# Kernel tuning notes

Hardware: AMD Instinct MI355X
Metric: run time of the kernel (lower is better)

The kernel has to match this reference:

```python
import jax, jax.numpy as jnp
import numpy as np

BETA = 0.05  # module hardcodes self.beta = 0.05 regardless of init arg
K = 4096
D = 512


def setup_inputs() -> dict:
    key = jax.random.key(0)
    k1, k2 = jax.random.split(key)
    latents = jax.random.normal(k1, (32, 1024, D), dtype=jnp.float32)
    # nn.Embedding weight init: normal_(mean=0.8, std=0.1)
    emb_weight = 0.8 + 0.1 * jax.random.normal(k2, (K, D), dtype=jnp.float32)
    return {"latents": latents, "emb_weight": emb_weight}


def reference(latents, emb_weight):
    B, S, Dm = latents.shape
    flat = latents.reshape(-1, Dm)  # [N, D]
    dist = (jnp.sum(flat * flat, axis=1, keepdims=True)
            + jnp.sum(emb_weight * emb_weight, axis=1)
            - 2.0 * jnp.matmul(flat, emb_weight.T))  # [N, K]
    inds = jnp.argmin(dist, axis=1)  # [N]
    quantized = emb_weight[inds].reshape(B, S, Dm)  # gather instead of one-hot matmul

    commitment_loss = jnp.mean((jax.lax.stop_gradient(quantized) - latents) ** 2)
    embedding_loss = jnp.mean((quantized - jax.lax.stop_gradient(latents)) ** 2)
    vq_loss = commitment_loss * BETA + embedding_loss

    # straight-through estimator
    quantized_st = latents + jax.lax.stop_gradient(quantized - latents)

    N = flat.shape[0]
    avg_probs = jnp.zeros((K,), dtype=latents.dtype).at[inds].add(1.0) / N
    perplexity = jnp.exp(-jnp.sum(avg_probs * jnp.log(avg_probs + 1e-10)))

    output_inds = inds.reshape(B, S)
    return (quantized_st, vq_loss, output_inds, emb_weight, perplexity)
```

## Files before the change

kernel.cpp:

```cpp
#include <hip/hip_runtime.h>
#include <cfloat>
#include <cmath>
#include <climits>
#include <cstdint>

#define N_ROWS   32768
#define D_DIM    512
#define K_CODES  4096

#define EPS_GAP  0.008f
#define CAND_WIN 0.02f
#define FLAG_CAP 12000

typedef short s16x8 __attribute__((ext_vector_type(8)));
typedef float f32x4 __attribute__((ext_vector_type(4)));


__device__ __forceinline__ short f2bf_rne(float x) {
    unsigned u = __float_as_uint(x);
    unsigned r = (u + 0x7fffu + ((u >> 16) & 1u)) >> 16;
    return (short)r;
}
__device__ __forceinline__ float bf2f(short b) {
    return __uint_as_float(((unsigned)(unsigned short)b) << 16);
}

__device__ __forceinline__ void gld16(const short* g, short* l) {
    __builtin_amdgcn_global_load_lds(
        reinterpret_cast<const __attribute__((address_space(1))) unsigned int*>(
            reinterpret_cast<uintptr_t>(g)),
        reinterpret_cast<__attribute__((address_space(3))) unsigned int*>(
            (unsigned int)(reinterpret_cast<uintptr_t>(l))),
        16, 0, 0);
}

__device__ __forceinline__ float np_block128_sq(const float* p) {
    float P[16];
    #pragma unroll
    for (int l = 0; l < 16; ++l) {
        float s0 = __fmul_rn(p[0 * 16 + l], p[0 * 16 + l]);
        float s1 = __fmul_rn(p[1 * 16 + l], p[1 * 16 + l]);
        float s2 = __fmul_rn(p[2 * 16 + l], p[2 * 16 + l]);
        float s3 = __fmul_rn(p[3 * 16 + l], p[3 * 16 + l]);
        float s4 = __fmul_rn(p[4 * 16 + l], p[4 * 16 + l]);
        float s5 = __fmul_rn(p[5 * 16 + l], p[5 * 16 + l]);
        float s6 = __fmul_rn(p[6 * 16 + l], p[6 * 16 + l]);
        float s7 = __fmul_rn(p[7 * 16 + l], p[7 * 16 + l]);
        float a01 = __fadd_rn(s0, s1);
        float a23 = __fadd_rn(s2, s3);
        float a45 = __fadd_rn(s4, s5);
        float a67 = __fadd_rn(s6, s7);
        P[l] = __fadd_rn(__fadd_rn(a01, a23), __fadd_rn(a45, a67));
    }
    float T3[8];
    #pragma unroll
    for (int k = 0; k < 8; ++k) T3[k] = __fadd_rn(P[k], P[k + 8]);
    float T6[4];
    #pragma unroll
    for (int k = 0; k < 4; ++k) T6[k] = __fadd_rn(T3[k], T3[k + 4]);
    return __fadd_rn(__fadd_rn(__fadd_rn(T6[0], T6[1]), T6[2]), T6[3]);
}
__device__ __forceinline__ float np_sum512_sq(const float* p) {
    float B0 = np_block128_sq(p);
    float B1 = np_block128_sq(p + 128);
    float B2 = np_block128_sq(p + 256);
    float B3 = np_block128_sq(p + 384);
    return __fadd_rn(__fadd_rn(B0, B1), __fadd_rn(B2, B3));
}

__global__ void vq_convert(const float* __restrict__ emb,
                           short* __restrict__ emb_hi, short* __restrict__ emb_lo) {
    int i = blockIdx.x * 256 + threadIdx.x;
    size_t base = (size_t)i * 8;
    float4 a = *(const float4*)(emb + base);
    float4 b = *(const float4*)(emb + base + 4);
    float x[8] = {a.x, a.y, a.z, a.w, b.x, b.y, b.z, b.w};
    s16x8 hv, lv;
    #pragma unroll
    for (int j = 0; j < 8; ++j) {
        short h = f2bf_rne(x[j]);
        hv[j] = h;
        lv[j] = f2bf_rne(x[j] - bf2f(h));
    }
    *(s16x8*)(emb_hi + base) = hv;
    *(s16x8*)(emb_lo + base) = lv;
}

__global__ void vq_enorm(const float* __restrict__ emb, float* __restrict__ e_norm) {
    int item = blockIdx.x * 4 + (threadIdx.x >> 6);
    int lane = threadIdx.x & 63;
    const float4* s4 = (const float4*)(emb + (size_t)item * D_DIM);
    float4 a = s4[lane];
    float4 b = s4[64 + lane];
    float s = a.x * a.x + a.y * a.y + a.z * a.z + a.w * a.w
            + b.x * b.x + b.y * b.y + b.z * b.z + b.w * b.w;
    #pragma unroll
    for (int off = 32; off > 0; off >>= 1) s += __shfl_down(s, off);
    if (lane == 0) e_norm[item] = s;
}

__device__ __forceinline__ int kswz(int r) { return (r & 3) ^ ((r >> 2) & 3); }

#define BROWS 256
#define BCOLS 256
#define KHALF 2048
#define BUFS2 32768

__global__ __launch_bounds__(1024, 4)
void vq_argmin_mfma(const float* __restrict__ lat,
                    const short* __restrict__ Bh_g, const short* __restrict__ Bl_g,
                    const float* __restrict__ e_norm,
                    float* __restrict__ pmin, float* __restrict__ psec,
                    unsigned short* __restrict__ pidx16)
{
    __shared__ short smem[2 * BUFS2];
    __shared__ float pbest_s[4][256];
    __shared__ float psec_s[4][256];
    __shared__ int   pidx_s[4][256];

    const int tid = threadIdx.x;
    const int l   = tid & 63;
    const int wid = tid >> 6;
    const int wr  = wid >> 2;
    const int wc  = wid & 3;
    const int l15 = l & 15;
    const int lhi = l >> 4;
    const int row0  = blockIdx.x * BROWS;
    const int kbase = blockIdx.y * KHALF;

    ((float*)pbest_s)[tid] = FLT_MAX;
    ((float*)psec_s)[tid]  = FLT_MAX;
    ((int*)pidx_s)[tid]    = 0;

    int offA[4], offB[4];
    #pragma unroll
    for (int m = 0; m < 4; ++m) {
        int r = wr * 64 + m * 16 + l15;
        offA[m] = r * 32 + (lhi ^ kswz(r)) * 8;
    }
    #pragma unroll
    for (int n = 0; n < 4; ++n) {
        int c = wc * 64 + n * 16 + l15;
        offB[n] = c * 32 + (lhi ^ kswz(c)) * 8;
    }

    const int ar = tid >> 2, asl = tid & 3;
    const int achunk = asl ^ kswz(ar);
    const size_t a_base = (size_t)(row0 + ar) * D_DIM + achunk * 8;
    const int adst = ar * 32 + asl * 8;
    const int br = tid >> 2, bsl = tid & 3;
    const int bchunk = bsl ^ kswz(br);
    const int bdst = tid * 8;

    {
        size_t go = (size_t)(kbase + br) * D_DIM + bchunk * 8;
        gld16(Bh_g + go, smem + 16384 + bdst);
        gld16(Bl_g + go, smem + 24576 + bdst);
        const float* p = lat + a_base;
        float4 f0 = *(const float4*)p;
        float4 f1 = *(const float4*)(p + 4);
        float x[8] = {f0.x, f0.y, f0.z, f0.w, f1.x, f1.y, f1.z, f1.w};
        s16x8 hv, lv;
        #pragma unroll
        for (int j = 0; j < 8; ++j) {
            short h = f2bf_rne(x[j]);
            hv[j] = h;
            lv[j] = f2bf_rne(x[j] - bf2f(h));
        }
        *(s16x8*)(smem + adst) = hv;
        *(s16x8*)(smem + 8192 + adst) = lv;
    }
    __syncthreads();

    f32x4 acc[4][4];
    #pragma unroll
    for (int m = 0; m < 4; ++m)
        #pragma unroll
        for (int n = 0; n < 4; ++n) acc[m][n] = (f32x4){0.f, 0.f, 0.f, 0.f};

    for (int s = 0; s < 128; ++s) {
        short* cur = smem + (s & 1) * BUFS2;
        short* nxt = smem + ((s & 1) ^ 1) * BUFS2;

        float4 nf0, nf1;
        if (s < 127) {
            const int s1 = s + 1;
            const int k0 = (s1 & 15) * 32;
            const float* p = lat + a_base + k0;
            nf0 = *(const float4*)p;
            nf1 = *(const float4*)(p + 4);
            size_t go = (size_t)(kbase + (s1 >> 4) * 256 + br) * D_DIM + k0 + bchunk * 8;
            gld16(Bh_g + go, nxt + 16384 + bdst);
            gld16(Bl_g + go, nxt + 24576 + bdst);
        }

        s16x8 ah[4], al[4];
        #pragma unroll
        for (int m = 0; m < 4; ++m) {
            ah[m] = *(const s16x8*)(cur + offA[m]);
            al[m] = *(const s16x8*)(cur + 8192 + offA[m]);
        }
        #pragma unroll
        for (int n = 0; n < 4; ++n) {
            s16x8 bh = *(const s16x8*)(cur + 16384 + offB[n]);
            s16x8 bl = *(const s16x8*)(cur + 24576 + offB[n]);
            #pragma unroll
            for (int m = 0; m < 4; ++m) {
                acc[m][n] = __builtin_amdgcn_mfma_f32_16x16x32_bf16(ah[m], bh, acc[m][n], 0, 0, 0);
                acc[m][n] = __builtin_amdgcn_mfma_f32_16x16x32_bf16(ah[m], bl, acc[m][n], 0, 0, 0);
                acc[m][n] = __builtin_amdgcn_mfma_f32_16x16x32_bf16(al[m], bh, acc[m][n], 0, 0, 0);
            }
        }

        if ((s & 15) == 15) {
            const int cb0 = kbase + (s >> 4) * 256;
            float en[4];
            int   cc[4];
            #pragma unroll
            for (int n = 0; n < 4; ++n) {
                cc[n] = cb0 + wc * 64 + n * 16 + l15;
                en[n] = e_norm[cc[n]];
            }
            #pragma unroll
            for (int m = 0; m < 4; ++m)
                #pragma unroll
                for (int r = 0; r < 4; ++r) {
                    float v = FLT_MAX, sc = FLT_MAX;
                    int ii = 0;
                    #pragma unroll
                    for (int n = 0; n < 4; ++n) {
                        float dv = __fmaf_rn(-2.f, acc[m][n][r], en[n]);
                        if (dv < v) { sc = v; v = dv; ii = cc[n]; }
                        else if (dv < sc) sc = dv;
                    }
                    #pragma unroll
                    for (int off = 8; off > 0; off >>= 1) {
                        float v2 = __shfl_xor(v, off);
                        float s2 = __shfl_xor(sc, off);
                        int   i2 = __shfl_xor(ii, off);
                        float ns = fminf(fminf(sc, s2), fmaxf(v, v2));
                        if (v2 < v || (v2 == v && i2 < ii)) { v = v2; ii = i2; }
                        sc = ns;
                    }
                    if (l15 == 0) {
                        int rb = wr * 64 + m * 16 + lhi * 4 + r;
                        float ob = pbest_s[wc][rb];
                        float os = psec_s[wc][rb];
                        float nsec = fminf(fminf(os, sc), fmaxf(ob, v));
                        if (v < ob) { pbest_s[wc][rb] = v; pidx_s[wc][rb] = ii; }
                        psec_s[wc][rb] = nsec;
                    }
                }
            #pragma unroll
            for (int m = 0; m < 4; ++m)
                #pragma unroll
                for (int n = 0; n < 4; ++n) acc[m][n] = (f32x4){0.f, 0.f, 0.f, 0.f};
        }

        if (s < 127) {
            float x[8] = {nf0.x, nf0.y, nf0.z, nf0.w, nf1.x, nf1.y, nf1.z, nf1.w};
            s16x8 hv, lv;
            #pragma unroll
            for (int j = 0; j < 8; ++j) {
                short h = f2bf_rne(x[j]);
                hv[j] = h;
                lv[j] = f2bf_rne(x[j] - bf2f(h));
            }
            *(s16x8*)(nxt + adst) = hv;
            *(s16x8*)(nxt + 8192 + adst) = lv;
        }
        __syncthreads();
    }

    if (tid < 256) {
        float B = FLT_MAX, S = FLT_MAX;
        int I = 0;
        #pragma unroll
        for (int w = 0; w < 4; ++w) {
            float b = pbest_s[w][tid], s = psec_s[w][tid];
            int i = pidx_s[w][tid];
            if (b < B || (b == B && i < I)) { S = fminf(B, s); B = b; I = i; }
            else S = fminf(S, fminf(b, s));
        }
        int row = row0 + tid;
        pmin[blockIdx.y * N_ROWS + row] = B;
        psec[blockIdx.y * N_ROWS + row] = S;
        pidx16[blockIdx.y * N_ROWS + row] = (unsigned short)I;
    }
}

__global__ void vq_select(const float* __restrict__ pmin, const float* __restrict__ psec,
                          const unsigned short* __restrict__ pidx16,
                          unsigned short* __restrict__ fidx, float* __restrict__ out_inds,
                          int* __restrict__ flagcnt, int* __restrict__ flaglist) {
    int row = blockIdx.x * 256 + threadIdx.x;
    float v0 = pmin[row], v1 = pmin[N_ROWS + row];
    float s0 = psec[row], s1 = psec[N_ROWS + row];
    int   i0 = pidx16[row], i1 = pidx16[N_ROWS + row];

    float best, sec; int bi;
    if (v1 < v0) { best = v1; bi = i1; sec = fminf(s1, v0); }
    else         { best = v0; bi = i0; sec = fminf(s0, v1); }

    fidx[row] = (unsigned short)bi;
    out_inds[row] = (float)bi;
    if (sec - best < EPS_GAP) {
        int p = atomicAdd(flagcnt, 1);
        if (p < FLAG_CAP) flaglist[p] = row;
    }
}

#define FIXT 1024
#define NWAV 16
#define MAXC 128

__global__ __launch_bounds__(FIXT)
void vq_fixrow(const float* __restrict__ lat, const float* __restrict__ emb,
               const int* __restrict__ flagcnt, const int* __restrict__ flaglist,
               unsigned short* __restrict__ fidx, float* __restrict__ out_inds)
{
    __shared__ float xs[D_DIM];
    __shared__ float dall[K_CODES];
    __shared__ float wmin_s[NWAV];
    __shared__ int   ccnt;
    __shared__ int   cands[MAXC];
    __shared__ float cd32[MAXC];

    const int t    = threadIdx.x;
    const int wave = t >> 6;
    const int lane = t & 63;
    int cnt = *flagcnt;
    if (cnt > FLAG_CAP) cnt = FLAG_CAP;

    for (int f = blockIdx.x; f < cnt; f += gridDim.x) {
        const int row = flaglist[f];
        __syncthreads();
        if (t < D_DIM) xs[t] = lat[(size_t)row * D_DIM + t];
        if (t == 0) ccnt = 0;
        __syncthreads();

        float x8[8];
        #pragma unroll
        for (int q = 0; q < 8; ++q) x8[q] = xs[lane * 8 + q];

        float lmin = FLT_MAX;
        for (int c = wave; c < K_CODES; c += 2 * NWAV) {
            const int c2 = c + NWAV;
            const float4* e4a = (const float4*)(emb + (size_t)c  * D_DIM);
            const float4* e4b = (const float4*)(emb + (size_t)c2 * D_DIM);
            float4 ea0 = e4a[lane * 2], ea1 = e4a[lane * 2 + 1];
            float4 eb0 = e4b[lane * 2], eb1 = e4b[lane * 2 + 1];

            float p0 = x8[0] - ea0.x, p1 = x8[1] - ea0.y;
            float p2 = x8[2] - ea0.z, p3 = x8[3] - ea0.w;
            float p4 = x8[4] - ea1.x, p5 = x8[5] - ea1.y;
            float p6 = x8[6] - ea1.z, p7 = x8[7] - ea1.w;
            float sA = __fmaf_rn(p0, p0, __fmaf_rn(p1, p1, __fmaf_rn(p2, p2, p3 * p3)));
            float sB = __fmaf_rn(p4, p4, __fmaf_rn(p5, p5, __fmaf_rn(p6, p6, p7 * p7)));
            float u = sA + sB;

            float q0 = x8[0] - eb0.x, q1 = x8[1] - eb0.y;
            float q2 = x8[2] - eb0.z, q3 = x8[3] - eb0.w;
            float q4 = x8[4] - eb1.x, q5 = x8[5] - eb1.y;
            float q6 = x8[6] - eb1.z, q7 = x8[7] - eb1.w;
            float tA = __fmaf_rn(q0, q0, __fmaf_rn(q1, q1, __fmaf_rn(q2, q2, q3 * q3)));
            float tB = __fmaf_rn(q4, q4, __fmaf_rn(q5, q5, __fmaf_rn(q6, q6, q7 * q7)));
            float v = tA + tB;

            #pragma unroll
            for (int off = 32; off > 0; off >>= 1) {
                u += __shfl_xor(u, off);
                v += __shfl_xor(v, off);
            }
            if (lane == 0) { dall[c] = u; dall[c2] = v; }
            lmin = fminf(lmin, fminf(u, v));
        }
        if (lane == 0) wmin_s[wave] = lmin;
        __syncthreads();

        float gmin = wmin_s[0];
        #pragma unroll
        for (int w = 1; w < NWAV; ++w) gmin = fminf(gmin, wmin_s[w]);
        const float thr = gmin + CAND_WIN;

        for (int c = t; c < K_CODES; c += FIXT) {
            if (dall[c] < thr) {
                int p = atomicAdd(&ccnt, 1);
                if (p < MAXC) cands[p] = c;
            }
        }
        __syncthreads();

        int nc = ccnt < MAXC ? ccnt : MAXC;
        if (t < nc) {
            int c = cands[t];
            const float* e = emb + (size_t)c * D_DIM;
            float t1 = np_sum512_sq(xs);
            float t2 = np_sum512_sq(e);
            float dot = 0.f;
            for (int k = 0; k < D_DIM; ++k)
                dot = __fmaf_rn(xs[k], e[k], dot);
            cd32[t] = __fsub_rn(__fadd_rn(t1, t2), __fmul_rn(2.f, dot));
        }
        __syncthreads();

        if (t == 0) {
            float bv = cd32[0]; int bx = cands[0];
            for (int w = 1; w < nc; ++w)
                if (cd32[w] < bv || (cd32[w] == bv && cands[w] < bx)) {
                    bv = cd32[w]; bx = cands[w];
                }
            fidx[row] = (unsigned short)bx;
            out_inds[row] = (float)bx;
        }
    }
}

__global__ void vq_gather(const float* __restrict__ lat, const float* __restrict__ emb,
                          const unsigned short* __restrict__ fidx,
                          float* __restrict__ out_q,
                          float* __restrict__ rowpart, int* __restrict__ hist) {
    int row  = blockIdx.x * 4 + (threadIdx.x >> 6);
    int lane = threadIdx.x & 63;
    int idx  = fidx[row];

    if (lane == 0) atomicAdd(&hist[idx], 1);

    const float4* e4 = (const float4*)(emb + (size_t)idx * D_DIM);
    const float4* x4 = (const float4*)(lat + (size_t)row * D_DIM);
    float4*       q4 = (float4*)(out_q + (size_t)row * D_DIM);

    float s = 0.f;
    #pragma unroll
    for (int i = 0; i < 2; ++i) {
        float4 e = e4[i * 64 + lane];
        float4 x = x4[i * 64 + lane];
        q4[i * 64 + lane] = e;
        float dx = e.x - x.x, dy = e.y - x.y, dz = e.z - x.z, dw = e.w - x.w;
        s += dx * dx + dy * dy + dz * dz + dw * dw;
    }
    #pragma unroll
    for (int off = 32; off > 0; off >>= 1) s += __shfl_down(s, off);
    if (lane == 0) rowpart[row] = s;
}

__global__ void vq_finalize(const float* __restrict__ rowpart, const int* __restrict__ hist,
                            float* __restrict__ out_loss, float* __restrict__ out_perp) {
    __shared__ float sdata[256];
    int t = threadIdx.x;

    float s = 0.f;
    for (int i = t; i < N_ROWS; i += 256) s += rowpart[i];
    sdata[t] = s;
    __syncthreads();
    for (int st = 128; st > 0; st >>= 1) {
        if (t < st) sdata[t] += sdata[t + st];
        __syncthreads();
    }
    if (t == 0) out_loss[0] = 1.05f * (sdata[0] / ((float)N_ROWS * (float)D_DIM));
    __syncthreads();

    float p = 0.f;
    for (int i = t; i < K_CODES; i += 256) {
        float pr = (float)hist[i] / (float)N_ROWS;
        p += pr * logf(pr + 1e-10f);
    }
    sdata[t] = p;
    __syncthreads();
    for (int st = 128; st > 0; st >>= 1) {
        if (t < st) sdata[t] += sdata[t + st];
        __syncthreads();
    }
    if (t == 0) out_perp[0] = expf(-sdata[0]);
}

extern "C" void kernel_launch(void* const* d_in, const int* in_sizes, int n_in,
                              void* d_out, int out_size, void* d_ws, size_t ws_size,
                              hipStream_t stream) {
    const float* lat = (const float*)d_in[0];
    const float* emb = (const float*)d_in[1];
    float* ob = (float*)d_out;

    short* emb_hi = (short*)(ob + 0);
    short* emb_lo = (short*)(ob + 1048576);
    float* pmin   = ob + 2097152;
    float* psec   = ob + 2162688;
    unsigned short* pidx16 = (unsigned short*)(ob + 2228224);
    float* e_norm = ob + 2260992;
    int*   flagcnt  = (int*)(ob + 2265088);
    int*   flaglist = (int*)(ob + 2265089);
    unsigned short* fidx = (unsigned short*)(ob + 16810000);
    int*   hist    = (int*)(ob + 16826384);
    float* rowpart = ob + 16830480;

    float* out_q    = ob;
    float* out_loss = ob + 16777216;
    float* out_inds = ob + 16777217;
    float* out_emb  = ob + 16809985;
    float* out_perp = ob + 18907137;

    hipMemsetAsync(flagcnt, 0, sizeof(int), stream);
    hipMemsetAsync(hist, 0, K_CODES * sizeof(int), stream);

    vq_convert<<<dim3(1024), dim3(256), 0, stream>>>(emb, emb_hi, emb_lo);
    vq_enorm<<<dim3(1024), dim3(256), 0, stream>>>(emb, e_norm);

    vq_argmin_mfma<<<dim3(N_ROWS / BROWS, 2), dim3(1024), 0, stream>>>(
        lat, emb_hi, emb_lo, e_norm, pmin, psec, pidx16);

    vq_select<<<dim3(N_ROWS / 256), dim3(256), 0, stream>>>(pmin, psec, pidx16,
                                                            fidx, out_inds,
                                                            flagcnt, flaglist);

    vq_fixrow<<<dim3(512), dim3(FIXT), 0, stream>>>(lat, emb, flagcnt, flaglist,
                                                    fidx, out_inds);

    vq_gather<<<dim3(N_ROWS / 4), dim3(256), 0, stream>>>(lat, emb, fidx, out_q, rowpart, hist);

    vq_finalize<<<dim3(1), dim3(256), 0, stream>>>(rowpart, hist, out_loss, out_perp);

    hipMemcpyAsync(out_emb, emb, (size_t)K_CODES * D_DIM * sizeof(float),
                   hipMemcpyDeviceToDevice, stream);
}
```

Before: 724.0 us.

## Fuse codebook convert and norm, truncate latent split, raise MFMA priority

Merges the codebook bf16 hi/lo conversion and the norm computation into one kernel, removing a launch and a second read of the codebook. The latent split inside the argmin kernel now truncates instead of rounding to nearest, which cuts integer ops per element. s_setprio is raised around the MFMA block to favour the issue of matrix instructions. Truncation makes the hi/lo split slightly less accurate and changes the summation order of e_norm, which may move near-tie rows relative to the rescoring tolerance.

Measured after the change: 705.9 us. 2.5% less time.

```diff
diff --git a/kernel.cpp b/kernel.cpp
--- a/kernel.cpp
+++ b/kernel.cpp
@@ -68,35 +68,29 @@
     return __fadd_rn(__fadd_rn(B0, B1), __fadd_rn(B2, B3));
 }
 
-__global__ void vq_convert(const float* __restrict__ emb,
-                           short* __restrict__ emb_hi, short* __restrict__ emb_lo) {
+__global__ void vq_conv_norm(const float* __restrict__ emb,
+                             short* __restrict__ emb_hi, short* __restrict__ emb_lo,
+                             float* __restrict__ e_norm) {
     int i = blockIdx.x * 256 + threadIdx.x;
+    int lane = threadIdx.x & 63;
     size_t base = (size_t)i * 8;
     float4 a = *(const float4*)(emb + base);
     float4 b = *(const float4*)(emb + base + 4);
     float x[8] = {a.x, a.y, a.z, a.w, b.x, b.y, b.z, b.w};
     s16x8 hv, lv;
+    float s = 0.f;
     #pragma unroll
     for (int j = 0; j < 8; ++j) {
         short h = f2bf_rne(x[j]);
         hv[j] = h;
         lv[j] = f2bf_rne(x[j] - bf2f(h));
+        s = __fmaf_rn(x[j], x[j], s);
     }
     *(s16x8*)(emb_hi + base) = hv;
     *(s16x8*)(emb_lo + base) = lv;
-}
-
-__global__ void vq_enorm(const float* __restrict__ emb, float* __restrict__ e_norm) {
-    int item = blockIdx.x * 4 + (threadIdx.x >> 6);
-    int lane = threadIdx.x & 63;
-    const float4* s4 = (const float4*)(emb + (size_t)item * D_DIM);
-    float4 a = s4[lane];
-    float4 b = s4[64 + lane];
-    float s = a.x * a.x + a.y * a.y + a.z * a.z + a.w * a.w
-            + b.x * b.x + b.y * b.y + b.z * b.z + b.w * b.w;
-    #pragma unroll
-    for (int off = 32; off > 0; off >>= 1) s += __shfl_down(s, off);
-    if (lane == 0) e_norm[item] = s;
+    #pragma unroll
+    for (int off = 32; off > 0; off >>= 1) s += __shfl_xor(s, off);
+    if (lane == 0) e_norm[i >> 6] = s;
 }
 
 __device__ __forceinline__ int kswz(int r) { return (r & 3) ^ ((r >> 2) & 3); }
@@ -105,6 +99,17 @@
 #define BCOLS 256
 #define KHALF 2048
 #define BUFS2 32768
+
+__device__ __forceinline__ void trunc_split8(const float* x, s16x8* hv, s16x8* lv) {
+    #pragma unroll
+    for (int j = 0; j < 8; ++j) {
+        unsigned ux = __float_as_uint(x[j]);
+        short h = (short)(ux >> 16);
+        (*hv)[j] = h;
+        float r = x[j] - bf2f(h);
+        (*lv)[j] = (short)(__float_as_uint(r) >> 16);
+    }
+}
 
 __global__ __launch_bounds__(1024, 4)
 void vq_argmin_mfma(const float* __restrict__ lat,
@@ -161,12 +166,7 @@
         float4 f1 = *(const float4*)(p + 4);
         float x[8] = {f0.x, f0.y, f0.z, f0.w, f1.x, f1.y, f1.z, f1.w};
         s16x8 hv, lv;
-        #pragma unroll
-        for (int j = 0; j < 8; ++j) {
-            short h = f2bf_rne(x[j]);
-            hv[j] = h;
-            lv[j] = f2bf_rne(x[j] - bf2f(h));
-        }
+        trunc_split8(x, &hv, &lv);
         *(s16x8*)(smem + adst) = hv;
         *(s16x8*)(smem + 8192 + adst) = lv;
     }
@@ -200,6 +200,7 @@
             ah[m] = *(const s16x8*)(cur + offA[m]);
             al[m] = *(const s16x8*)(cur + 8192 + offA[m]);
         }
+        __builtin_amdgcn_s_setprio(1);
         #pragma unroll
         for (int n = 0; n < 4; ++n) {
             s16x8 bh = *(const s16x8*)(cur + 16384 + offB[n]);
@@ -211,6 +212,7 @@
                 acc[m][n] = __builtin_amdgcn_mfma_f32_16x16x32_bf16(al[m], bh, acc[m][n], 0, 0, 0);
             }
         }
+        __builtin_amdgcn_s_setprio(0);
 
         if ((s & 15) == 15) {
             const int cb0 = kbase + (s >> 4) * 256;
@@ -260,12 +262,7 @@
         if (s < 127) {
             float x[8] = {nf0.x, nf0.y, nf0.z, nf0.w, nf1.x, nf1.y, nf1.z, nf1.w};
             s16x8 hv, lv;
-            #pragma unroll
-            for (int j = 0; j < 8; ++j) {
-                short h = f2bf_rne(x[j]);
-                hv[j] = h;
-                lv[j] = f2bf_rne(x[j] - bf2f(h));
-            }
+            trunc_split8(x, &hv, &lv);
             *(s16x8*)(nxt + adst) = hv;
             *(s16x8*)(nxt + 8192 + adst) = lv;
         }
@@ -502,8 +499,7 @@
     hipMemsetAsync(flagcnt, 0, sizeof(int), stream);
     hipMemsetAsync(hist, 0, K_CODES * sizeof(int), stream);
 
-    vq_convert<<<dim3(1024), dim3(256), 0, stream>>>(emb, emb_hi, emb_lo);
-    vq_enorm<<<dim3(1024), dim3(256), 0, stream>>>(emb, e_norm);
+    vq_conv_norm<<<dim3(1024), dim3(256), 0, stream>>>(emb, emb_hi, emb_lo, e_norm);
 
     vq_argmin_mfma<<<dim3(N_ROWS / BROWS, 2), dim3(1024), 0, stream>>>(
         lat, emb_hi, emb_lo, e_norm, pmin, psec, pidx16);
```
